# Performance work log

Hardware: AMD Instinct MI355X
Metric: run time of the kernel (lower is better)

## Reference

```python
import jax, jax.numpy as jnp
import numpy as np

N_NODES = 100000
N_EDGES = 1600000
D = 128
NUM_EXPERTS = 8
NUM_LAYERS = 2
EPS = 1e-5


def setup_inputs() -> dict:
    key = jax.random.key(0)
    ks = jax.random.split(key, 8)
    x = jax.random.normal(ks[0], (N_NODES, D), dtype=jnp.float32)
    edge_index = jax.random.randint(ks[1], (2, N_EDGES), 0, N_NODES, dtype=jnp.int64)
    # weights scaled for sane numerics (like torch default inits)
    W_self = jax.random.normal(ks[2], (NUM_EXPERTS, NUM_LAYERS, D, D), dtype=jnp.float32) * 0.05
    W_nbr = jax.random.normal(ks[3], (NUM_EXPERTS, NUM_LAYERS, D, D), dtype=jnp.float32) * 0.05
    b = jax.random.normal(ks[4], (NUM_EXPERTS, NUM_LAYERS, D), dtype=jnp.float32) * 0.05
    gamma = jnp.ones((NUM_EXPERTS, NUM_LAYERS - 1, D), dtype=jnp.float32)
    beta = jnp.zeros((NUM_EXPERTS, NUM_LAYERS - 1, D), dtype=jnp.float32)
    return {"x": x, "edge_index": edge_index, "W_self": W_self, "W_nbr": W_nbr,
            "b": b, "gamma": gamma, "beta": beta}


def _sage_encoder(x, src, dst, inv_deg, W_self, W_nbr, b, gamma, beta):
    # One GraphSAGE-style encoder: per layer, mean-aggregate neighbor feats,
    # transform self + neighbor, then BatchNorm + ReLU (all but last layer).
    h = x
    for l in range(NUM_LAYERS):
        agg = jax.ops.segment_sum(h[src], dst, num_segments=N_NODES) * inv_deg  # [N, d]
        h = h @ W_self[l] + agg @ W_nbr[l] + b[l]
        if l < NUM_LAYERS - 1:
            mean = jnp.mean(h, axis=0)
            var = jnp.var(h, axis=0)
            h = gamma[l] * (h - mean) * jax.lax.rsqrt(var + EPS) + beta[l]
            h = jax.nn.relu(h)
        # dropout: identity in inference mode
    return h  # [N, d]


def reference(x, edge_index, W_self, W_nbr, b, gamma, beta):
    src, dst = edge_index[0], edge_index[1]
    deg = jax.ops.segment_sum(jnp.ones((N_EDGES,), x.dtype), dst, num_segments=N_NODES)
    inv_deg = (1.0 / jnp.maximum(deg, 1.0))[:, None]  # [N, 1]
    outs = [
        _sage_encoder(x, src, dst, inv_deg, W_self[e], W_nbr[e], b[e], gamma[e], beta[e])
        for e in range(NUM_EXPERTS)
    ]
    return jnp.stack(outs, axis=-1)  # [N, hidden, num_experts]
```

## Files before the change

kernel.cpp:

```cpp
#include <hip/hip_runtime.h>
#include <stdint.h>

#define NN 100000
#define NED 1600000
#define DD 128
#define NE 8
#define ND ((size_t)NN * (size_t)DD)
#define BNEPS 1e-5f

typedef __attribute__((ext_vector_type(8))) short short8;
typedef __attribute__((ext_vector_type(4))) float float4v;

__device__ __forceinline__ float bf2f(uint32_t h) {
    union { uint32_t u; float f; } c; c.u = h << 16; return c.f;
}
__device__ __forceinline__ uint16_t f2bf(float x) {
    union { float f; uint32_t u; } c; c.f = x;
    uint32_t r = (c.u + 0x7fffu + ((c.u >> 16) & 1u)) >> 16;
    return (uint16_t)r;
}

__global__ __launch_bounds__(256) void k_deg(const int* __restrict__ dst, int* __restrict__ deg) {
    int i = blockIdx.x * 256 + threadIdx.x;
    int stride = gridDim.x * 256;
    for (; i < NED; i += stride) atomicAdd(&deg[dst[i]], 1);
}

__global__ __launch_bounds__(1024) void k_scan1(const int* __restrict__ deg, int* __restrict__ rp,
                                                int* __restrict__ bsum) {
    __shared__ int sh[1024];
    int t = threadIdx.x;
    int i = blockIdx.x * 1024 + t;
    int v = (i < NN) ? deg[i] : 0;
    sh[t] = v; __syncthreads();
    for (int off = 1; off < 1024; off <<= 1) {
        int add = (t >= off) ? sh[t - off] : 0;
        __syncthreads();
        sh[t] += add;
        __syncthreads();
    }
    if (i < NN) rp[i] = sh[t] - v;
    if (t == 1023) bsum[blockIdx.x] = sh[1023];
}

__global__ void k_scan2(int* bsum) {
    if (threadIdx.x == 0) {
        int acc = 0;
        for (int j = 0; j < 98; ++j) { int t = bsum[j]; bsum[j] = acc; acc += t; }
    }
}

__global__ __launch_bounds__(1024) void k_scan3(const int* __restrict__ deg, int* __restrict__ rp,
                                                const int* __restrict__ bsum, int* __restrict__ cur,
                                                float* __restrict__ invd) {
    int i = blockIdx.x * 1024 + threadIdx.x;
    if (i == 0) rp[NN] = NED;
    if (i < NN) {
        int r = rp[i] + bsum[blockIdx.x];
        rp[i] = r; cur[i] = r;
        invd[i] = 1.0f / fmaxf((float)deg[i], 1.0f);
    }
}

__global__ __launch_bounds__(256) void k_scatter(const int* __restrict__ src, const int* __restrict__ dst,
                                                 int* __restrict__ cur, int* __restrict__ esrc) {
    int i = blockIdx.x * 256 + threadIdx.x;
    int stride = gridDim.x * 256;
    for (; i < NED; i += stride) {
        int d = dst[i];
        int p = atomicAdd(&cur[d], 1);
        esrc[p] = src[i];
    }
}

__global__ __launch_bounds__(256) void k_castx(const float* __restrict__ x, uint16_t* __restrict__ xb) {
    size_t i = ((size_t)blockIdx.x * 256 + threadIdx.x) * 8;
    if (i >= ND) return;
    float4 a = *(const float4*)(x + i);
    float4 b = *(const float4*)(x + i + 4);
    uint4 u;
    u.x = (uint32_t)f2bf(a.x) | ((uint32_t)f2bf(a.y) << 16);
    u.y = (uint32_t)f2bf(a.z) | ((uint32_t)f2bf(a.w) << 16);
    u.z = (uint32_t)f2bf(b.x) | ((uint32_t)f2bf(b.y) << 16);
    u.w = (uint32_t)f2bf(b.z) | ((uint32_t)f2bf(b.w) << 16);
    *(uint4*)(xb + i) = u;
}

__global__ __launch_bounds__(256) void k_agg(const uint16_t* __restrict__ srcf, uint16_t* __restrict__ dstf,
                                             size_t estride, const int* __restrict__ rp,
                                             const int* __restrict__ esrc, const float* __restrict__ invd) {
    const uint16_t* sp = srcf + (size_t)blockIdx.y * estride;
    uint16_t* dp = dstf + (size_t)blockIdx.y * estride;
    int wave = threadIdx.x >> 6, lane = threadIdx.x & 63;
    int node = blockIdx.x * 4 + wave;
    if (node >= NN) return;
    int beg = rp[node], end = rp[node + 1];
    float s0 = 0, s1 = 0, t0 = 0, t1 = 0;
    int i = beg;
    for (; i + 1 < end; i += 2) {
        int a = esrc[i], b = esrc[i + 1];
        uint32_t va = *(const uint32_t*)(sp + (size_t)a * DD + lane * 2);
        uint32_t vb = *(const uint32_t*)(sp + (size_t)b * DD + lane * 2);
        s0 += bf2f(va & 0xffff); s1 += bf2f(va >> 16);
        t0 += bf2f(vb & 0xffff); t1 += bf2f(vb >> 16);
    }
    if (i < end) {
        int a = esrc[i];
        uint32_t va = *(const uint32_t*)(sp + (size_t)a * DD + lane * 2);
        s0 += bf2f(va & 0xffff); s1 += bf2f(va >> 16);
    }
    float id = invd[node];
    s0 = (s0 + t0) * id; s1 = (s1 + t1) * id;
    uint32_t pk = (uint32_t)f2bf(s0) | ((uint32_t)f2bf(s1) << 16);
    *(uint32_t*)(dp + (size_t)node * DD + lane * 2) = pk;
}

__global__ __launch_bounds__(256, 2) void k_gemm(
    const float* __restrict__ Wself, const float* __restrict__ Wnbr, const float* __restrict__ bglob,
    int layer, int e0,
    const uint16_t* __restrict__ A1, const uint16_t* __restrict__ A2, size_t a_estride,
    uint16_t* __restrict__ outb, size_t o_zstride, int out_mode, float* __restrict__ outf) {
    __shared__ __align__(16) uint16_t wlds[128 * 256];
    int tid = threadIdx.x;
    int bz = blockIdx.z;
    int e = e0 + bz;
    size_t wbase = ((size_t)e * 2 + layer) * (128 * 128);

    for (int i = tid; i < 128 * 32; i += 256) {
        int n = i & 127, g = i >> 7;
        uint16_t tmp[8];
#pragma unroll
        for (int j = 0; j < 8; ++j) {
            int k = g * 8 + j;
            float w = (k < 128) ? Wself[wbase + (size_t)k * 128 + n]
                                : Wnbr[wbase + (size_t)(k - 128) * 128 + n];
            tmp[j] = f2bf(w);
        }
        uint4 u;
        u.x = (uint32_t)tmp[0] | ((uint32_t)tmp[1] << 16);
        u.y = (uint32_t)tmp[2] | ((uint32_t)tmp[3] << 16);
        u.z = (uint32_t)tmp[4] | ((uint32_t)tmp[5] << 16);
        u.w = (uint32_t)tmp[6] | ((uint32_t)tmp[7] << 16);
        *(uint4*)&wlds[n * 256 + (((g ^ n) & 31) << 3)] = u;
    }
    __syncthreads();

    const uint16_t* A1p = A1 + (size_t)bz * a_estride;
    const uint16_t* A2p = A2 + (size_t)bz * a_estride;

    int wave = tid >> 6, lane = tid & 63;
    int m = lane & 15, quad = lane >> 4;
    int rowBase = blockIdx.x * 256 + wave * 64;

    float4v acc[4][8];
#pragma unroll
    for (int rt = 0; rt < 4; ++rt)
#pragma unroll
        for (int nt = 0; nt < 8; ++nt)
            acc[rt][nt] = (float4v){0.f, 0.f, 0.f, 0.f};

#pragma unroll
    for (int ks = 0; ks < 8; ++ks) {
        int kk = ks * 32 + quad * 8;
        short8 af[4];
#pragma unroll
        for (int rt = 0; rt < 4; ++rt) {
            int row = rowBase + rt * 16 + m;
            row = row < NN ? row : NN - 1;
            const uint16_t* ap = (kk < 128) ? (A1p + (size_t)row * DD + kk)
                                            : (A2p + (size_t)row * DD + (kk - 128));
            af[rt] = *(const short8*)ap;
        }
        int g = kk >> 3;
#pragma unroll
        for (int nt = 0; nt < 8; ++nt) {
            int n = nt * 16 + m;
            short8 bf = *(const short8*)&wlds[n * 256 + (((g ^ n) & 31) << 3)];
#pragma unroll
            for (int rt = 0; rt < 4; ++rt)
                acc[rt][nt] = __builtin_amdgcn_mfma_f32_16x16x32_bf16(af[rt], bf, acc[rt][nt], 0, 0, 0);
        }
    }

    size_t bofs = ((size_t)e * 2 + layer) * 128;
    size_t zoffb = (out_mode == 1) ? (size_t)e * ND : (size_t)bz * o_zstride;
#pragma unroll
    for (int rt = 0; rt < 4; ++rt) {
#pragma unroll
        for (int nt = 0; nt < 8; ++nt) {
            int col = nt * 16 + m;
            float bv = bglob[bofs + col];
#pragma unroll
            for (int r = 0; r < 4; ++r) {
                int row = rowBase + rt * 16 + quad * 4 + r;
                if (row < NN) {
                    float v = acc[rt][nt][r] + bv;
                    if (out_mode == 2) outf[(size_t)row * 1024 + col * 8 + e] = v;
                    else outb[zoffb + (size_t)row * DD + col] = f2bf(v);
                }
            }
        }
    }
}

__global__ __launch_bounds__(256) void k_stats(const uint16_t* __restrict__ H, size_t estride, int e0,
                                               float* __restrict__ stats) {
    int e = e0 + blockIdx.y;
    const uint16_t* Hp = H + (size_t)blockIdx.y * estride;
    int f = threadIdx.x & 127, half = threadIdx.x >> 7;
    float s = 0, ss = 0;
    for (int row = blockIdx.x * 2 + half; row < NN; row += gridDim.x * 2) {
        float v = bf2f(Hp[(size_t)row * DD + f]);
        s += v; ss += v * v;
    }
    __shared__ float sh[512];
    sh[threadIdx.x] = s; sh[256 + threadIdx.x] = ss;
    __syncthreads();
    if (half == 0) {
        float st = sh[f] + sh[128 + f];
        float sq = sh[256 + f] + sh[256 + 128 + f];
        atomicAdd(&stats[e * 256 + f], st);
        atomicAdd(&stats[e * 256 + 128 + f], sq);
    }
}

__global__ void k_coef(const float* __restrict__ stats, const float* __restrict__ gamma,
                       const float* __restrict__ beta, int e0, float* __restrict__ coef) {
    int e = e0 + blockIdx.x;
    int f = threadIdx.x;
    float s = stats[e * 256 + f], ss = stats[e * 256 + 128 + f];
    float mean = s / (float)NN;
    float var = ss / (float)NN - mean * mean;
    float sc = gamma[e * 128 + f] * rsqrtf(var + BNEPS);
    coef[e * 256 + f] = sc;
    coef[e * 256 + 128 + f] = beta[e * 128 + f] - mean * sc;
}

__global__ __launch_bounds__(256) void k_affine(uint16_t* __restrict__ H, size_t estride, int e0,
                                                const float* __restrict__ coef) {
    int e = e0 + blockIdx.y;
    uint16_t* Hp = H + (size_t)blockIdx.y * estride;
    const float* sc = coef + e * 256;
    const float* sf = sc + 128;
    size_t i = ((size_t)blockIdx.x * 256 + threadIdx.x) * 8;
    if (i >= ND) return;
    int f = (int)(i & 127);
    uint4 u = *(const uint4*)(Hp + i);
    uint32_t w[4] = {u.x, u.y, u.z, u.w};
    uint32_t o[4];
#pragma unroll
    for (int j = 0; j < 4; ++j) {
        float v0 = fmaxf(bf2f(w[j] & 0xffff) * sc[f + 2 * j] + sf[f + 2 * j], 0.f);
        float v1 = fmaxf(bf2f(w[j] >> 16) * sc[f + 2 * j + 1] + sf[f + 2 * j + 1], 0.f);
        o[j] = (uint32_t)f2bf(v0) | ((uint32_t)f2bf(v1) << 16);
    }
    uint4 ou = {o[0], o[1], o[2], o[3]};
    *(uint4*)(Hp + i) = ou;
}

__global__ __launch_bounds__(256) void k_transpose(const uint16_t* __restrict__ O, float* __restrict__ out) {
    size_t t = (size_t)blockIdx.x * 256 + threadIdx.x;
    if (t >= ND / 2) return;
    size_t idx = t * 2;
    float v0[8], v1[8];
#pragma unroll
    for (int e = 0; e < 8; ++e) {
        uint32_t u = *(const uint32_t*)(O + (size_t)e * ND + idx);
        v0[e] = bf2f(u & 0xffff); v1[e] = bf2f(u >> 16);
    }
    float* op = out + idx * 8;
    float4 a = {v0[0], v0[1], v0[2], v0[3]}, b = {v0[4], v0[5], v0[6], v0[7]};
    float4 c = {v1[0], v1[1], v1[2], v1[3]}, d = {v1[4], v1[5], v1[6], v1[7]};
    *(float4*)(op) = a; *(float4*)(op + 4) = b; *(float4*)(op + 8) = c; *(float4*)(op + 12) = d;
}

extern "C" void kernel_launch(void* const* d_in, const int* in_sizes, int n_in,
                              void* d_out, int out_size, void* d_ws, size_t ws_size,
                              hipStream_t stream) {
    const float* x = (const float*)d_in[0];
    const int* ei = (const int*)d_in[1];
    const float* Wself = (const float*)d_in[2];
    const float* Wnbr = (const float*)d_in[3];
    const float* bias = (const float*)d_in[4];
    const float* gamma = (const float*)d_in[5];
    const float* beta = (const float*)d_in[6];
    float* out = (float*)d_out;
    const int* src = ei;
    const int* dst = ei + NED;

    char* ws = (char*)d_ws;
    size_t off = 0;
    auto alloc = [&](size_t b) { size_t p = off; off += (b + 255) & ~(size_t)255; return p; };
    int* deg = (int*)(ws + alloc((size_t)NN * 4));
    int* rp = (int*)(ws + alloc((size_t)(NN + 1) * 4));
    int* cur = (int*)(ws + alloc((size_t)NN * 4));
    int* esrc = (int*)(ws + alloc((size_t)NED * 4));
    float* invd = (float*)(ws + alloc((size_t)NN * 4));
    int* bsum = (int*)(ws + alloc(98 * 4));
    float* stats = (float*)(ws + alloc(NE * 256 * 4));
    float* coef = (float*)(ws + alloc(NE * 256 * 4));
    uint16_t* xb = (uint16_t*)(ws + alloc(ND * 2));
    uint16_t* agg0 = (uint16_t*)(ws + alloc(ND * 2));

    size_t rem = (ws_size > off) ? ws_size - off : 0;
    size_t plane = ND * 2;
    bool batched, useO;
    if (rem >= 24 * plane + 4096) { batched = true; useO = true; }
    else if (rem >= 10 * plane + 4096) { batched = false; useO = true; }
    else { batched = false; useO = false; }

    uint16_t* H = (uint16_t*)(ws + alloc((batched ? NE : 1) * plane));
    uint16_t* A2 = (uint16_t*)(ws + alloc((batched ? NE : 1) * plane));
    uint16_t* Otmp = useO ? (uint16_t*)(ws + alloc((size_t)NE * plane)) : nullptr;

    hipMemsetAsync(deg, 0, (size_t)NN * 4, stream);
    hipMemsetAsync(stats, 0, NE * 256 * 4, stream);

    k_deg<<<2048, 256, 0, stream>>>(dst, deg);
    k_scan1<<<98, 1024, 0, stream>>>(deg, rp, bsum);
    k_scan2<<<1, 64, 0, stream>>>(bsum);
    k_scan3<<<98, 1024, 0, stream>>>(deg, rp, bsum, cur, invd);
    k_scatter<<<2048, 256, 0, stream>>>(src, dst, cur, esrc);
    k_castx<<<6250, 256, 0, stream>>>(x, xb);
    k_agg<<<dim3(25000, 1), 256, 0, stream>>>(xb, agg0, 0, rp, esrc, invd);

    int gz = batched ? NE : 1;
    size_t estride = batched ? ND : 0;
    int nloop = batched ? 1 : NE;
    for (int e = 0; e < nloop; ++e) {
        int e0 = batched ? 0 : e;
        k_gemm<<<dim3(391, 1, gz), 256, 0, stream>>>(Wself, Wnbr, bias, 0, e0,
                                                     xb, agg0, 0, H, estride, 0, nullptr);
        k_stats<<<dim3(500, gz), 256, 0, stream>>>(H, estride, e0, stats);
        k_coef<<<gz, 128, 0, stream>>>(stats, gamma, beta, e0, coef);
        k_affine<<<dim3(6250, gz), 256, 0, stream>>>(H, estride, e0, coef);
        k_agg<<<dim3(25000, gz), 256, 0, stream>>>(H, A2, estride, rp, esrc, invd);
        if (useO)
            k_gemm<<<dim3(391, 1, gz), 256, 0, stream>>>(Wself, Wnbr, bias, 1, e0,
                                                         H, A2, estride, Otmp, 0, 1, nullptr);
        else
            k_gemm<<<dim3(391, 1, gz), 256, 0, stream>>>(Wself, Wnbr, bias, 1, e0,
                                                         H, A2, estride, nullptr, 0, 2, out);
    }
    if (useO) k_transpose<<<25000, 256, 0, stream>>>(Otmp, out);
}
```

Before: 2.183 ms.

## Interleave expert hidden states per node and aggregate all experts in one gather

Layer-1 hidden states for all eight experts are now stored node-major as [N, 8, 128] bf16, so each node's 1024 features sit in one contiguous 2 KB row. A new k_agg8 kernel gathers each neighbor's full row with 16-byte loads, covering all experts in one pass over the CSR edge list instead of eight separate passes. It writes with nontemporal stores. The GEMM, stats and affine kernels take the interleaved stride, and the non-batched fallback path is dropped, so the workspace must now hold all expert planes. The cost is 16 fp32 accumulators per lane and strided GEMM A-loads.

```diff
diff --git a/kernel.cpp b/kernel.cpp
--- a/kernel.cpp
+++ b/kernel.cpp
@@ -6,10 +6,12 @@
 #define DD 128
 #define NE 8
 #define ND ((size_t)NN * (size_t)DD)
+#define NDE (ND * NE)
 #define BNEPS 1e-5f
 
 typedef __attribute__((ext_vector_type(8))) short short8;
 typedef __attribute__((ext_vector_type(4))) float float4v;
+typedef __attribute__((ext_vector_type(4))) unsigned int uint4v;
 
 __device__ __forceinline__ float bf2f(uint32_t h) {
     union { uint32_t u; float f; } c; c.u = h << 16; return c.f;
@@ -86,11 +88,9 @@
     *(uint4*)(xb + i) = u;
 }
 
-__global__ __launch_bounds__(256) void k_agg(const uint16_t* __restrict__ srcf, uint16_t* __restrict__ dstf,
-                                             size_t estride, const int* __restrict__ rp,
-                                             const int* __restrict__ esrc, const float* __restrict__ invd) {
-    const uint16_t* sp = srcf + (size_t)blockIdx.y * estride;
-    uint16_t* dp = dstf + (size_t)blockIdx.y * estride;
+__global__ __launch_bounds__(256) void k_agg(const uint16_t* __restrict__ sp, uint16_t* __restrict__ dp,
+                                             const int* __restrict__ rp, const int* __restrict__ esrc,
+                                             const float* __restrict__ invd) {
     int wave = threadIdx.x >> 6, lane = threadIdx.x & 63;
     int node = blockIdx.x * 4 + wave;
     if (node >= NN) return;
@@ -105,25 +105,71 @@
         t0 += bf2f(vb & 0xffff); t1 += bf2f(vb >> 16);
     }
     if (i < end) {
-        int a = esrc[i];
-        uint32_t va = *(const uint32_t*)(sp + (size_t)a * DD + lane * 2);
+        uint32_t va = *(const uint32_t*)(sp + (size_t)esrc[i] * DD + lane * 2);
         s0 += bf2f(va & 0xffff); s1 += bf2f(va >> 16);
     }
     float id = invd[node];
     s0 = (s0 + t0) * id; s1 = (s1 + t1) * id;
-    uint32_t pk = (uint32_t)f2bf(s0) | ((uint32_t)f2bf(s1) << 16);
-    *(uint32_t*)(dp + (size_t)node * DD + lane * 2) = pk;
+    *(uint32_t*)(dp + (size_t)node * DD + lane * 2) = (uint32_t)f2bf(s0) | ((uint32_t)f2bf(s1) << 16);
+}
+
+__device__ __forceinline__ void acc_u4(float* a, uint4 u) {
+    a[0] += bf2f(u.x & 0xffffu); a[1] += bf2f(u.x >> 16);
+    a[2] += bf2f(u.y & 0xffffu); a[3] += bf2f(u.y >> 16);
+    a[4] += bf2f(u.z & 0xffffu); a[5] += bf2f(u.z >> 16);
+    a[6] += bf2f(u.w & 0xffffu); a[7] += bf2f(u.w >> 16);
+}
+
+__global__ __launch_bounds__(256) void k_agg8(const uint16_t* __restrict__ Hi,
+                                              uint16_t* __restrict__ A2i,
+                                              const int* __restrict__ rp,
+                                              const int* __restrict__ esrc,
+                                              const float* __restrict__ invd) {
+    int wave = threadIdx.x >> 6, lane = threadIdx.x & 63;
+    int node = blockIdx.x * 4 + wave;
+    if (node >= NN) return;
+    int beg = rp[node], end = rp[node + 1];
+    float acc[16];
+#pragma unroll
+    for (int j = 0; j < 16; ++j) acc[j] = 0.f;
+    const size_t loff = (size_t)(lane * 16);
+    int i = beg;
+    for (; i + 1 < end; i += 2) {
+        const uint16_t* pa = Hi + (size_t)esrc[i] * 1024 + loff;
+        const uint16_t* pb = Hi + (size_t)esrc[i + 1] * 1024 + loff;
+        uint4 a0 = *(const uint4*)pa;
+        uint4 a1 = *(const uint4*)(pa + 8);
+        uint4 b0 = *(const uint4*)pb;
+        uint4 b1 = *(const uint4*)(pb + 8);
+        acc_u4(acc, a0); acc_u4(acc + 8, a1);
+        acc_u4(acc, b0); acc_u4(acc + 8, b1);
+    }
+    if (i < end) {
+        const uint16_t* pa = Hi + (size_t)esrc[i] * 1024 + loff;
+        uint4 a0 = *(const uint4*)pa;
+        uint4 a1 = *(const uint4*)(pa + 8);
+        acc_u4(acc, a0); acc_u4(acc + 8, a1);
+    }
+    float id = invd[node];
+    uint32_t pk[8];
+#pragma unroll
+    for (int j = 0; j < 8; ++j)
+        pk[j] = (uint32_t)f2bf(acc[2 * j] * id) | ((uint32_t)f2bf(acc[2 * j + 1] * id) << 16);
+    uint4v o0 = {pk[0], pk[1], pk[2], pk[3]};
+    uint4v o1 = {pk[4], pk[5], pk[6], pk[7]};
+    uint16_t* dp = A2i + (size_t)node * 1024 + loff;
+    __builtin_nontemporal_store(o0, (uint4v*)dp);
+    __builtin_nontemporal_store(o1, (uint4v*)(dp + 8));
 }
 
 __global__ __launch_bounds__(256, 2) void k_gemm(
     const float* __restrict__ Wself, const float* __restrict__ Wnbr, const float* __restrict__ bglob,
-    int layer, int e0,
-    const uint16_t* __restrict__ A1, const uint16_t* __restrict__ A2, size_t a_estride,
-    uint16_t* __restrict__ outb, size_t o_zstride, int out_mode, float* __restrict__ outf) {
+    int layer,
+    const uint16_t* __restrict__ A1, const uint16_t* __restrict__ A2, int a_rstride, int a_ezoff,
+    uint16_t* __restrict__ outb, int out_mode, float* __restrict__ outf) {
     __shared__ __align__(16) uint16_t wlds[128 * 256];
     int tid = threadIdx.x;
-    int bz = blockIdx.z;
-    int e = e0 + bz;
+    int e = blockIdx.z;
     size_t wbase = ((size_t)e * 2 + layer) * (128 * 128);
 
     for (int i = tid; i < 128 * 32; i += 256) {
@@ -145,8 +191,8 @@
     }
     __syncthreads();
 
-    const uint16_t* A1p = A1 + (size_t)bz * a_estride;
-    const uint16_t* A2p = A2 + (size_t)bz * a_estride;
+    const uint16_t* A1p = A1 + (size_t)e * a_ezoff;
+    const uint16_t* A2p = A2 + (size_t)e * a_ezoff;
 
     int wave = tid >> 6, lane = tid & 63;
     int m = lane & 15, quad = lane >> 4;
@@ -167,8 +213,8 @@
         for (int rt = 0; rt < 4; ++rt) {
             int row = rowBase + rt * 16 + m;
             row = row < NN ? row : NN - 1;
-            const uint16_t* ap = (kk < 128) ? (A1p + (size_t)row * DD + kk)
-                                            : (A2p + (size_t)row * DD + (kk - 128));
+            const uint16_t* ap = (kk < 128) ? (A1p + (size_t)row * a_rstride + kk)
+                                            : (A2p + (size_t)row * a_rstride + (kk - 128));
             af[rt] = *(const short8*)ap;
         }
         int g = kk >> 3;
@@ -183,7 +229,6 @@
     }
 
     size_t bofs = ((size_t)e * 2 + layer) * 128;
-    size_t zoffb = (out_mode == 1) ? (size_t)e * ND : (size_t)bz * o_zstride;
 #pragma unroll
     for (int rt = 0; rt < 4; ++rt) {
 #pragma unroll
@@ -195,38 +240,36 @@
                 int row = rowBase + rt * 16 + quad * 4 + r;
                 if (row < NN) {
                     float v = acc[rt][nt][r] + bv;
-                    if (out_mode == 2) outf[(size_t)row * 1024 + col * 8 + e] = v;
-                    else outb[zoffb + (size_t)row * DD + col] = f2bf(v);
+                    if (out_mode == 0) outb[(size_t)row * 1024 + (size_t)e * 128 + col] = f2bf(v);
+                    else if (out_mode == 1) outb[(size_t)e * ND + (size_t)row * DD + col] = f2bf(v);
+                    else outf[(size_t)row * 1024 + col * 8 + e] = v;
                 }
             }
         }
     }
 }
 
-__global__ __launch_bounds__(256) void k_stats(const uint16_t* __restrict__ H, size_t estride, int e0,
-                                               float* __restrict__ stats) {
-    int e = e0 + blockIdx.y;
-    const uint16_t* Hp = H + (size_t)blockIdx.y * estride;
+__global__ __launch_bounds__(256) void k_stats(const uint16_t* __restrict__ H, float* __restrict__ stats) {
+    int e = blockIdx.y;
+    const uint16_t* Hp = H + e * 128;
     int f = threadIdx.x & 127, half = threadIdx.x >> 7;
     float s = 0, ss = 0;
     for (int row = blockIdx.x * 2 + half; row < NN; row += gridDim.x * 2) {
-        float v = bf2f(Hp[(size_t)row * DD + f]);
+        float v = bf2f(Hp[(size_t)row * 1024 + f]);
         s += v; ss += v * v;
     }
     __shared__ float sh[512];
     sh[threadIdx.x] = s; sh[256 + threadIdx.x] = ss;
     __syncthreads();
     if (half == 0) {
-        float st = sh[f] + sh[128 + f];
-        float sq = sh[256 + f] + sh[256 + 128 + f];
-        atomicAdd(&stats[e * 256 + f], st);
-        atomicAdd(&stats[e * 256 + 128 + f], sq);
+        atomicAdd(&stats[e * 256 + f], sh[f] + sh[128 + f]);
+        atomicAdd(&stats[e * 256 + 128 + f], sh[256 + f] + sh[256 + 128 + f]);
     }
 }
 
 __global__ void k_coef(const float* __restrict__ stats, const float* __restrict__ gamma,
-                       const float* __restrict__ beta, int e0, float* __restrict__ coef) {
-    int e = e0 + blockIdx.x;
+                       const float* __restrict__ beta, float* __restrict__ coef) {
+    int e = blockIdx.x;
     int f = threadIdx.x;
     float s = stats[e * 256 + f], ss = stats[e * 256 + 128 + f];
     float mean = s / (float)NN;
@@ -236,26 +279,24 @@
     coef[e * 256 + 128 + f] = beta[e * 128 + f] - mean * sc;
 }
 
-__global__ __launch_bounds__(256) void k_affine(uint16_t* __restrict__ H, size_t estride, int e0,
-                                                const float* __restrict__ coef) {
-    int e = e0 + blockIdx.y;
-    uint16_t* Hp = H + (size_t)blockIdx.y * estride;
+__global__ __launch_bounds__(256) void k_affine(uint16_t* __restrict__ H, const float* __restrict__ coef) {
+    size_t i = ((size_t)blockIdx.x * 256 + threadIdx.x) * 8;
+    if (i >= NDE) return;
+    int e = (int)((i >> 7) & 7);
+    int ff = (int)(i & 127);
     const float* sc = coef + e * 256;
     const float* sf = sc + 128;
-    size_t i = ((size_t)blockIdx.x * 256 + threadIdx.x) * 8;
-    if (i >= ND) return;
-    int f = (int)(i & 127);
-    uint4 u = *(const uint4*)(Hp + i);
+    uint4 u = *(const uint4*)(H + i);
     uint32_t w[4] = {u.x, u.y, u.z, u.w};
     uint32_t o[4];
 #pragma unroll
     for (int j = 0; j < 4; ++j) {
-        float v0 = fmaxf(bf2f(w[j] & 0xffff) * sc[f + 2 * j] + sf[f + 2 * j], 0.f);
-        float v1 = fmaxf(bf2f(w[j] >> 16) * sc[f + 2 * j + 1] + sf[f + 2 * j + 1], 0.f);
+        float v0 = fmaxf(bf2f(w[j] & 0xffffu) * sc[ff + 2 * j] + sf[ff + 2 * j], 0.f);
+        float v1 = fmaxf(bf2f(w[j] >> 16) * sc[ff + 2 * j + 1] + sf[ff + 2 * j + 1], 0.f);
         o[j] = (uint32_t)f2bf(v0) | ((uint32_t)f2bf(v1) << 16);
     }
     uint4 ou = {o[0], o[1], o[2], o[3]};
-    *(uint4*)(Hp + i) = ou;
+    *(uint4*)(H + i) = ou;
 }
 
 __global__ __launch_bounds__(256) void k_transpose(const uint16_t* __restrict__ O, float* __restrict__ out) {
@@ -304,13 +345,10 @@
 
     size_t rem = (ws_size > off) ? ws_size - off : 0;
     size_t plane = ND * 2;
-    bool batched, useO;
-    if (rem >= 24 * plane + 4096) { batched = true; useO = true; }
-    else if (rem >= 10 * plane + 4096) { batched = false; useO = true; }
-    else { batched = false; useO = false; }
-
-    uint16_t* H = (uint16_t*)(ws + alloc((batched ? NE : 1) * plane));
-    uint16_t* A2 = (uint16_t*)(ws + alloc((batched ? NE : 1) * plane));
+    bool useO = rem >= 24 * plane + 4096;
+
+    uint16_t* Hi = (uint16_t*)(ws + alloc(NE * plane));
+    uint16_t* A2i = (uint16_t*)(ws + alloc(NE * plane));
     uint16_t* Otmp = useO ? (uint16_t*)(ws + alloc((size_t)NE * plane)) : nullptr;
 
     hipMemsetAsync(deg, 0, (size_t)NN * 4, stream);
@@ -322,25 +360,23 @@
     k_scan3<<<98, 1024, 0, stream>>>(deg, rp, bsum, cur, invd);
     k_scatter<<<2048, 256, 0, stream>>>(src, dst, cur, esrc);
     k_castx<<<6250, 256, 0, stream>>>(x, xb);
-    k_agg<<<dim3(25000, 1), 256, 0, stream>>>(xb, agg0, 0, rp, esrc, invd);
-
-    int gz = batched ? NE : 1;
-    size_t estride = batched ? ND : 0;
-    int nloop = batched ? 1 : NE;
-    for (int e = 0; e < nloop; ++e) {
-        int e0 = batched ? 0 : e;
-        k_gemm<<<dim3(391, 1, gz), 256, 0, stream>>>(Wself, Wnbr, bias, 0, e0,
-                                                     xb, agg0, 0, H, estride, 0, nullptr);
-        k_stats<<<dim3(500, gz), 256, 0, stream>>>(H, estride, e0, stats);
-        k_coef<<<gz, 128, 0, stream>>>(stats, gamma, beta, e0, coef);
-        k_affine<<<dim3(6250, gz), 256, 0, stream>>>(H, estride, e0, coef);
-        k_agg<<<dim3(25000, gz), 256, 0, stream>>>(H, A2, estride, rp, esrc, invd);
-        if (useO)
-            k_gemm<<<dim3(391, 1, gz), 256, 0, stream>>>(Wself, Wnbr, bias, 1, e0,
-                                                         H, A2, estride, Otmp, 0, 1, nullptr);
-        else
-            k_gemm<<<dim3(391, 1, gz), 256, 0, stream>>>(Wself, Wnbr, bias, 1, e0,
-                                                         H, A2, estride, nullptr, 0, 2, out);
-    }
-    if (useO) k_transpose<<<25000, 256, 0, stream>>>(Otmp, out);
-}
+
+    k_agg<<<25000, 256, 0, stream>>>(xb, agg0, rp, esrc, invd);
+
+    k_gemm<<<dim3(391, 1, NE), 256, 0, stream>>>(Wself, Wnbr, bias, 0,
+                                                 xb, agg0, 128, 0, Hi, 0, nullptr);
+    k_stats<<<dim3(500, NE), 256, 0, stream>>>(Hi, stats);
+    k_coef<<<NE, 128, 0, stream>>>(stats, gamma, beta, coef);
+    k_affine<<<50000, 256, 0, stream>>>(Hi, coef);
+
+    k_agg8<<<25000, 256, 0, stream>>>(Hi, A2i, rp, esrc, invd);
+
+    if (useO) {
+        k_gemm<<<dim3(391, 1, NE), 256, 0, stream>>>(Wself, Wnbr, bias, 1,
+                                                     Hi, A2i, 1024, 128, Otmp, 1, nullptr);
+        k_transpose<<<25000, 256, 0, stream>>>(Otmp, out);
+    } else {
+        k_gemm<<<dim3(391, 1, NE), 256, 0, stream>>>(Wself, Wnbr, bias, 1,
+                                                     Hi, A2i, 1024, 128, nullptr, 2, out);
+    }
+}
```

New measurement: 1.973 ms. -9.6%, faster.
